# Performance work log

Hardware: AMD Instinct MI355X
Metric: run time of the kernel (lower is better)

Reference implementation:

```python
import jax, jax.numpy as jnp
import numpy as np

EPS = 1e-5  # torch LayerNorm default

def _ln(x, g, b):
    m = x.mean(-1, keepdims=True)
    v = x.var(-1, keepdims=True)  # biased var, matches torch LayerNorm
    return (x - m) * jax.lax.rsqrt(v + EPS) * g + b

def setup_inputs() -> dict:
    key = jax.random.key(0)
    ks = jax.random.split(key, 8)
    B, T, D, H, depth, C = 64, 512, 1024, 1024, 2, 1024
    return {
        'input': jax.random.normal(ks[0], (B, T, D), jnp.float32),
        'w_ih': jax.random.normal(ks[1], (depth, 4 * H, D), jnp.float32),
        'b_ih': jax.random.normal(ks[2], (depth, 4 * H), jnp.float32),
        'w_hh': jax.random.normal(ks[3], (depth, 4 * H, H), jnp.float32),
        'b_hh': jax.random.normal(ks[4], (depth, 4 * H), jnp.float32),
        'g_ih': jax.random.uniform(ks[5], (depth, 4 * H), jnp.float32),
        'be_ih': jnp.zeros((depth, 4 * H), jnp.float32),
        'g_hh': jax.random.uniform(ks[6], (depth, 4 * H), jnp.float32),
        'be_hh': jnp.zeros((depth, 4 * H), jnp.float32),
        'g_ho': jax.random.uniform(ks[7], (depth, H), jnp.float32),
        'be_ho': jnp.zeros((depth, H), jnp.float32),
        'fc_w': jax.random.normal(jax.random.fold_in(key, 9), (C, H), jnp.float32),
        'fc_b': jnp.zeros((C,), jnp.float32),
    }

def reference(input, w_ih, b_ih, w_hh, b_hh, g_ih, be_ih, g_hh, be_hh, g_ho, be_ho, fc_w, fc_b):
    B, T, D = input.shape
    depth, four_h, H = w_hh.shape
    H = four_h // 4
    h0 = jnp.zeros((depth, B, H), input.dtype)
    c0 = jnp.zeros((depth, B, H), input.dtype)
    xs = jnp.swapaxes(input, 0, 1)  # [T, B, D]

    def step(carry, x_t):
        h, c = carry
        x = x_t
        new_h, new_c = [], []
        for l in range(depth):  # small fixed layer loop
            gates = (_ln(x @ w_ih[l].T + b_ih[l], g_ih[l], be_ih[l])
                     + _ln(h[l] @ w_hh[l].T + b_hh[l], g_hh[l], be_hh[l]))  # [B, 4H]
            i, f, o = jnp.split(jax.nn.sigmoid(gates[:, :3 * H]), 3, axis=1)
            g = jnp.tanh(gates[:, 3 * H:])
            cy = f * c[l] + i * g
            hy = o * jnp.tanh(_ln(cy, g_ho[l], be_ho[l]))
            new_h.append(hy)
            new_c.append(cy)
            x = hy
        return (jnp.stack(new_h), jnp.stack(new_c)), x

    _, ys = jax.lax.scan(step, (h0, c0), xs)  # ys: [T, B, H] (top-layer h)
    out = jnp.swapaxes(ys, 0, 1).reshape(B * T, H) @ fc_w.T + fc_b
    return out.reshape(B, T, -1)
```

## Files before the change

### kernel.cpp

```cpp
#include <hip/hip_runtime.h>


typedef __attribute__((ext_vector_type(8))) short short8;
typedef __attribute__((ext_vector_type(8))) __bf16 bf16x8;
typedef __attribute__((ext_vector_type(4))) float f32x4;
typedef __attribute__((ext_vector_type(4))) unsigned short us4;

#define B_ 64
#define T_ 512
#define D_ 1024
#define H_ 1024
#define FH_ 4096
#define LAG_ 16
#define NS_ (T_ + LAG_)
#define RCH_ (B_ * 16)

typedef const __attribute__((address_space(1))) unsigned int* gas_ptr;
typedef __attribute__((address_space(3))) unsigned int* las_ptr;
#define GLOAD_LDS16(g, l) \
  __builtin_amdgcn_global_load_lds((gas_ptr)(g), (las_ptr)(l), 16, 0, 0)

static __device__ __forceinline__ unsigned short f2bf(float f) {
  unsigned int u = __builtin_bit_cast(unsigned int, f);
  u += 0x7FFFu + ((u >> 16) & 1u);
  return (unsigned short)(u >> 16);
}
static __device__ __forceinline__ float bf2f(unsigned short u) {
  unsigned int x = ((unsigned int)u) << 16;
  return __builtin_bit_cast(float, x);
}

__global__ void cast_split_k(const float4* __restrict__ in,
                             us4* __restrict__ hi, us4* __restrict__ lo, int n4) {
  int i = blockIdx.x * 256 + threadIdx.x;
  if (i < n4) {
    float4 v = in[i];
    us4 h, l;
    h[0] = f2bf(v.x); l[0] = f2bf(v.x - bf2f(h[0]));
    h[1] = f2bf(v.y); l[1] = f2bf(v.y - bf2f(h[1]));
    h[2] = f2bf(v.z); l[2] = f2bf(v.z - bf2f(h[2]));
    h[3] = f2bf(v.w); l[3] = f2bf(v.w - bf2f(h[3]));
    hi[i] = h; lo[i] = l;
  }
}

__global__ void transpose_split_k(const float4* __restrict__ x,
                                  us4* __restrict__ hi, us4* __restrict__ lo) {
  int i = blockIdx.x * 256 + threadIdx.x;
  int d4  = i & 255;
  int rem = i >> 8;
  int b = rem & 63;
  int t = rem >> 6;
  float4 v = x[((size_t)(b * T_ + t) << 8) + d4];
  us4 h, l;
  h[0] = f2bf(v.x); l[0] = f2bf(v.x - bf2f(h[0]));
  h[1] = f2bf(v.y); l[1] = f2bf(v.y - bf2f(h[1]));
  h[2] = f2bf(v.z); l[2] = f2bf(v.z - bf2f(h[2]));
  h[3] = f2bf(v.w); l[3] = f2bf(v.w - bf2f(h[3]));
  size_t o = ((size_t)(t * B_ + b) << 8) + d4;
  hi[o] = h; lo[o] = l;
}

__global__ void whh_frag_k(const float* __restrict__ w_hh,
                           unsigned short* __restrict__ frag) {
  int i = blockIdx.x * 256 + threadIdx.x;
  int sl   = i >> 12;
  int rem  = i & 4095;
  int sel  = rem >> 11;
  int kc   = (rem >> 6) & 31;
  int lane = rem & 63;
  int layer = sl >> 8, j = sl & 255;
  int col = j * 16 + (lane & 15);
  int kof = kc * 32 + (lane >> 4) * 8;
  const float* src = w_hh + ((size_t)layer * FH_ + col) * 1024 + kof;
  short8 o;
#pragma unroll
  for (int e = 0; e < 8; ++e) {
    float v = src[e];
    unsigned short h = f2bf(v);
    o[e] = sel ? (short)f2bf(v - bf2f(h)) : (short)h;
  }
  *(short8*)(frag + (size_t)i * 8) = o;
}

template <int FCMODE>
__global__ __launch_bounds__(256) void gemm3_k(
    const unsigned short* __restrict__ Ahi, const unsigned short* __restrict__ Alo,
    const unsigned short* __restrict__ Whi, const unsigned short* __restrict__ Wlo,
    const float* __restrict__ bias, float* __restrict__ out, int K, int N) {
  __shared__ unsigned short lAh[128 * 40];
  __shared__ unsigned short lAl[128 * 40];
  __shared__ unsigned short lWh[128 * 40];
  __shared__ unsigned short lWl[128 * 40];
  int tid = threadIdx.x;
  int l = tid & 63, w = tid >> 6;
  int r0 = blockIdx.y * 128, c0 = blockIdx.x * 128;
  int wr = (w >> 1) * 64, wc = (w & 1) * 64;
  int lr = l & 15, lk = (l >> 4) * 8;
  f32x4 acc[4][4] = {};
  int srow = tid >> 2;
  int scc  = (tid & 3) * 8;

  for (int kt = 0; kt < K; kt += 32) {
#pragma unroll
    for (int i = 0; i < 2; ++i) {
      int row = srow + i * 64;
      size_t aoff = (size_t)(r0 + row) * K + kt + scc;
      size_t woff = (size_t)(c0 + row) * K + kt + scc;
      *(short8*)&lAh[row * 40 + scc] = *(const short8*)(Ahi + aoff);
      *(short8*)&lAl[row * 40 + scc] = *(const short8*)(Alo + aoff);
      *(short8*)&lWh[row * 40 + scc] = *(const short8*)(Whi + woff);
      *(short8*)&lWl[row * 40 + scc] = *(const short8*)(Wlo + woff);
    }
    __syncthreads();
    bf16x8 ah[4], al[4], bh[4], bl[4];
#pragma unroll
    for (int mi = 0; mi < 4; ++mi) {
      ah[mi] = *(bf16x8*)&lAh[(wr + mi * 16 + lr) * 40 + lk];
      al[mi] = *(bf16x8*)&lAl[(wr + mi * 16 + lr) * 40 + lk];
    }
#pragma unroll
    for (int ni = 0; ni < 4; ++ni) {
      bh[ni] = *(bf16x8*)&lWh[(wc + ni * 16 + lr) * 40 + lk];
      bl[ni] = *(bf16x8*)&lWl[(wc + ni * 16 + lr) * 40 + lk];
    }
#pragma unroll
    for (int mi = 0; mi < 4; ++mi)
#pragma unroll
      for (int ni = 0; ni < 4; ++ni) {
        acc[mi][ni] = __builtin_amdgcn_mfma_f32_16x16x32_bf16(ah[mi], bh[ni], acc[mi][ni], 0, 0, 0);
        acc[mi][ni] = __builtin_amdgcn_mfma_f32_16x16x32_bf16(ah[mi], bl[ni], acc[mi][ni], 0, 0, 0);
        acc[mi][ni] = __builtin_amdgcn_mfma_f32_16x16x32_bf16(al[mi], bh[ni], acc[mi][ni], 0, 0, 0);
      }
    __syncthreads();
  }

#pragma unroll
  for (int mi = 0; mi < 4; ++mi)
#pragma unroll
    for (int ni = 0; ni < 4; ++ni)
#pragma unroll
      for (int reg = 0; reg < 4; ++reg) {
        int r = r0 + wr + mi * 16 + (l >> 4) * 4 + reg;
        int c = c0 + wc + ni * 16 + lr;
        float v = acc[mi][ni][reg] + bias[c];
        if (FCMODE) {
          int b = r & 63, t = r >> 6;
          out[((size_t)b * T_ + t) * (size_t)N + c] = v;
        } else {
          out[(size_t)r * N + c] = v;
        }
      }
}

__global__ __launch_bounds__(256) void hh_lds_k(
    const unsigned short* __restrict__ hH, const unsigned short* __restrict__ hL,
    const unsigned short* __restrict__ whhFrag,
    float* __restrict__ G, int s) {
  int layer = blockIdx.x >> 8;
  int t = layer ? (s - LAG_) : s;
  if (t < 0 || t >= T_) return;
  int j = blockIdx.x & 255;
  extern __shared__ char smem[];
  unsigned short* wl = (unsigned short*)smem;
  int tid = threadIdx.x;
  int l = tid & 63, w = tid >> 6;
  int lr = l & 15, lk = (l >> 4) * 8, lq = l >> 4;

  const unsigned short* gsrc = whhFrag + (((size_t)(layer * 256 + j)) << 15);
#pragma unroll
  for (int r = 0; r < 16; ++r) {
    int c = r * 256 + tid;
    GLOAD_LDS16(gsrc + (size_t)c * 8, wl + (size_t)(r * 256 + w * 64) * 8);
  }

  const unsigned short* hHb = hH + layer * 65536;
  const unsigned short* hLb = hL + layer * 65536;
  int m0 = w * 16;

  __syncthreads();

  f32x4 acc = {};
#pragma unroll 8
  for (int kc = 0; kc < 32; ++kc) {
    int k = kc * 32 + lk;
    bf16x8 ah = __builtin_bit_cast(bf16x8, *(const short8*)(hHb + (m0 + lr) * 1024 + k));
    bf16x8 al = __builtin_bit_cast(bf16x8, *(const short8*)(hLb + (m0 + lr) * 1024 + k));
    bf16x8 bh = __builtin_bit_cast(bf16x8, *(const short8*)&wl[(size_t)(kc * 64 + l) * 8]);
    bf16x8 bl = __builtin_bit_cast(bf16x8, *(const short8*)&wl[(size_t)(2048 + kc * 64 + l) * 8]);
    acc = __builtin_amdgcn_mfma_f32_16x16x32_bf16(ah, bh, acc, 0, 0, 0);
    acc = __builtin_amdgcn_mfma_f32_16x16x32_bf16(ah, bl, acc, 0, 0, 0);
    acc = __builtin_amdgcn_mfma_f32_16x16x32_bf16(al, bh, acc, 0, 0, 0);
  }
  float* Gb = G + layer * (64 * FH_);
  int n0 = j * 16;
#pragma unroll
  for (int reg = 0; reg < 4; ++reg) {
    int row = m0 + lq * 4 + reg;
    Gb[(size_t)row * FH_ + n0 + lr] = acc[reg];
  }
}

__device__ __forceinline__ void wave_red(float& v) {
#pragma unroll
  for (int o = 32; o; o >>= 1) v += __shfl_down(v, o);
}

__global__ __launch_bounds__(256) void pointwise_k(
    const float* __restrict__ P0, const float* __restrict__ P1,
    const float* __restrict__ G,
    const float* __restrict__ b_hh, const float* __restrict__ g_ih,
    const float* __restrict__ be_ih, const float* __restrict__ g_hh,
    const float* __restrict__ be_hh, const float* __restrict__ g_ho,
    const float* __restrict__ be_ho,
    float* __restrict__ cst,
    unsigned short* __restrict__ hH, unsigned short* __restrict__ hL,
    unsigned short* __restrict__ XYhi, unsigned short* __restrict__ XYlo,
    int s) {
  int layer = blockIdx.x >> 6;
  int t = layer ? (s - LAG_) : s;
  if (t < 0 || t >= T_) return;
  __shared__ float red[16];
  int r = blockIdx.x & 63, j = threadIdx.x;
  int wv = j >> 6, ln = j & 63;
  int slot = s & 15;
  const float* Pr = (layer ? P1 : P0) + ((size_t)slot * B_ + r) * FH_;
  const float* Gr = G + layer * (64 * FH_) + (size_t)r * FH_;
  const float* bhh = b_hh + layer * FH_;
  const float* gih = g_ih + layer * FH_;
  const float* beih= be_ih + layer * FH_;
  const float* ghh = g_hh + layer * FH_;
  const float* behh= be_hh + layer * FH_;
  const float* gho = g_ho + layer * H_;
  const float* beho= be_ho + layer * H_;
  float* crow = cst + layer * 65536 + (size_t)r * H_;

  float ihp[16], hhp[16];
  float s1 = 0, q1 = 0, s2 = 0, q2 = 0;
#pragma unroll
  for (int st = 0; st < 16; ++st) {
    int n = j + 256 * st;
    float a = Pr[n];
    float b = Gr[n] + bhh[n];
    ihp[st] = a; hhp[st] = b;
    s1 += a; q1 += a * a; s2 += b; q2 += b * b;
  }
  wave_red(s1); wave_red(q1); wave_red(s2); wave_red(q2);
  if (ln == 0) { red[wv * 4] = s1; red[wv * 4 + 1] = q1; red[wv * 4 + 2] = s2; red[wv * 4 + 3] = q2; }
  __syncthreads();
  s1 = red[0] + red[4] + red[8] + red[12];
  q1 = red[1] + red[5] + red[9] + red[13];
  s2 = red[2] + red[6] + red[10] + red[14];
  q2 = red[3] + red[7] + red[11] + red[15];
  __syncthreads();

  const float inv4h = 1.0f / 4096.0f;
  float m1 = s1 * inv4h, m2 = s2 * inv4h;
  float i1 = rsqrtf(q1 * inv4h - m1 * m1 + 1e-5f);
  float i2 = rsqrtf(q2 * inv4h - m2 * m2 + 1e-5f);

  float pre[16];
#pragma unroll
  for (int st = 0; st < 16; ++st) {
    int n = j + 256 * st;
    pre[st] = gih[n] * (ihp[st] - m1) * i1 + beih[n] + ghh[n] * (hhp[st] - m2) * i2 + behh[n];
  }

  float cn[4], og[4];
  float s3 = 0, q3 = 0;
#pragma unroll
  for (int u = 0; u < 4; ++u) {
    int hidx = j + 256 * u;
    float iG = 1.0f / (1.0f + __expf(-pre[u]));
    float fG = 1.0f / (1.0f + __expf(-pre[u + 4]));
    float oG = 1.0f / (1.0f + __expf(-pre[u + 8]));
    float gG = tanhf(pre[u + 12]);
    float c = fG * crow[hidx] + iG * gG;
    crow[hidx] = c;
    cn[u] = c; og[u] = oG;
    s3 += c; q3 += c * c;
  }
  wave_red(s3); wave_red(q3);
  if (ln == 0) { red[wv * 4] = s3; red[wv * 4 + 1] = q3; }
  __syncthreads();
  s3 = red[0] + red[4] + red[8] + red[12];
  q3 = red[1] + red[5] + red[9] + red[13];

  const float invh = 1.0f / 1024.0f;
  float m3 = s3 * invh;
  float i3 = rsqrtf(q3 * invh - m3 * m3 + 1e-5f);
  unsigned short* hHb = hH + layer * 65536 + (size_t)r * H_;
  unsigned short* hLb = hL + layer * 65536 + (size_t)r * H_;
  unsigned short* YH = XYhi + ((size_t)t * B_ + r) * H_;
  unsigned short* YL = XYlo + ((size_t)t * B_ + r) * H_;
#pragma unroll
  for (int u = 0; u < 4; ++u) {
    int hidx = j + 256 * u;
    float hy = og[u] * tanhf((cn[u] - m3) * i3 * gho[hidx] + beho[hidx]);
    unsigned short hv = f2bf(hy);
    unsigned short lv = f2bf(hy - bf2f(hv));
    hHb[hidx] = hv; hLb[hidx] = lv;
    YH[hidx] = hv;  YL[hidx] = lv;
  }
}

extern "C" void kernel_launch(void* const* d_in, const int* in_sizes, int n_in,
                              void* d_out, int out_size, void* d_ws, size_t ws_size,
                              hipStream_t stream) {
  const float* x    = (const float*)d_in[0];
  const float* w_ih = (const float*)d_in[1];
  const float* b_ih = (const float*)d_in[2];
  const float* w_hh = (const float*)d_in[3];
  const float* b_hh = (const float*)d_in[4];
  const float* g_ih = (const float*)d_in[5];
  const float* be_ih= (const float*)d_in[6];
  const float* g_hh = (const float*)d_in[7];
  const float* be_hh= (const float*)d_in[8];
  const float* g_ho = (const float*)d_in[9];
  const float* be_ho= (const float*)d_in[10];
  const float* fc_w = (const float*)d_in[11];
  const float* fc_b = (const float*)d_in[12];
  float* out = (float*)d_out;
  (void)ws_size; (void)in_sizes; (void)n_in; (void)out_size;

  char* wsb = (char*)d_ws;
  size_t off = 0;
  unsigned short* wihHi  = (unsigned short*)(wsb + off); off += 16777216;
  unsigned short* wihLo  = (unsigned short*)(wsb + off); off += 16777216;
  unsigned short* whhFrag= (unsigned short*)(wsb + off); off += 33554432;
  unsigned short* fcHi   = (unsigned short*)(wsb + off); off += 2097152;
  unsigned short* fcLo   = (unsigned short*)(wsb + off); off += 2097152;
  unsigned short* XYhi   = (unsigned short*)(wsb + off); off += 67108864;
  unsigned short* XYlo   = (unsigned short*)(wsb + off); off += 67108864;
  float* P0              = (float*)(wsb + off); off += (size_t)16 * B_ * FH_ * 4;
  float* P1              = (float*)(wsb + off); off += (size_t)16 * B_ * FH_ * 4;
  float* G               = (float*)(wsb + off); off += (size_t)2 * B_ * FH_ * 4;
  unsigned short* hH     = (unsigned short*)(wsb + off); off += 262144;
  unsigned short* hL     = (unsigned short*)(wsb + off); off += 262144;
  float* cst             = (float*)(wsb + off); off += 524288;

  {
    int n4 = 2 * FH_ * D_ / 4;
    cast_split_k<<<(n4 + 255) / 256, 256, 0, stream>>>((const float4*)w_ih, (us4*)wihHi, (us4*)wihLo, n4);
    int nf = H_ * H_ / 4;
    cast_split_k<<<(nf + 255) / 256, 256, 0, stream>>>((const float4*)fc_w, (us4*)fcHi, (us4*)fcLo, nf);
    int nx = T_ * B_ * D_ / 4;
    transpose_split_k<<<nx / 256, 256, 0, stream>>>((const float4*)x, (us4*)XYhi, (us4*)XYlo);
    whh_frag_k<<<8192, 256, 0, stream>>>(w_hh, whhFrag);
  }

  hipMemsetAsync(hH, 0, 262144, stream);
  hipMemsetAsync(hL, 0, 262144, stream);
  hipMemsetAsync(cst, 0, 524288, stream);

  hipFuncSetAttribute(reinterpret_cast<const void*>(hh_lds_k),
                      hipFuncAttributeMaxDynamicSharedMemorySize, 65536);

  for (int s = 0; s < NS_; ++s) {
    if ((s & 15) == 0) {
      if (s < T_) {
        gemm3_k<0><<<dim3(FH_ / 128, RCH_ / 128), 256, 0, stream>>>(
            XYhi + (size_t)s * B_ * D_, XYlo + (size_t)s * B_ * D_,
            wihHi, wihLo, b_ih, P0, D_, FH_);
      }
      if (s >= LAG_) {
        gemm3_k<0><<<dim3(FH_ / 128, RCH_ / 128), 256, 0, stream>>>(
            XYhi + (size_t)(s - LAG_) * B_ * D_, XYlo + (size_t)(s - LAG_) * B_ * D_,
            wihHi + (1 << 22), wihLo + (1 << 22), b_ih + FH_, P1, D_, FH_);
      }
    }
    hh_lds_k<<<512, 256, 65536, stream>>>(hH, hL, whhFrag, G, s);
    pointwise_k<<<128, 256, 0, stream>>>(P0, P1, G, b_hh, g_ih, be_ih, g_hh, be_hh,
                                         g_ho, be_ho, cst, hH, hL, XYhi, XYlo, s);
  }

  gemm3_k<1><<<dim3(H_ / 128, (T_ * B_) / 128), 256, 0, stream>>>(
      XYhi, XYlo, fcHi, fcLo, fc_b, out, H_, H_);
}
```

Measured before the change: 17.99 ms.

## Fuse recurrent matmul and pointwise LSTM step into one cooperative kernel

Replaces the per-step hh GEMM kernel and the pointwise LayerNorm/gate kernel with a single cooperative kernel of 256 blocks. Each block owns 8 hidden columns across all four gates, so the gate preactivations stay in LDS and the G buffer round trip disappears. Row LayerNorm statistics are combined across blocks with global atomics, separated by two software grid barriers. The intent is to remove one launch per step and the global traffic for G, at the cost of barrier spin latency, atomic contention, and a larger LDS footprint per block.

```diff
diff --git a/kernel.cpp b/kernel.cpp
--- a/kernel.cpp
+++ b/kernel.cpp
@@ -14,6 +14,9 @@
 #define LAG_ 16
 #define NS_ (T_ + LAG_)
 #define RCH_ (B_ * 16)
+
+#define SMEM_WHH 131072
+#define SMEM_TOTAL (SMEM_WHH + 64 * 33 * 4)
 
 typedef const __attribute__((address_space(1))) unsigned int* gas_ptr;
 typedef __attribute__((address_space(3))) unsigned int* las_ptr;
@@ -61,18 +64,19 @@
   hi[o] = h; lo[o] = l;
 }
 
-__global__ void whh_frag_k(const float* __restrict__ w_hh,
-                           unsigned short* __restrict__ frag) {
+__global__ void whh_frag3_k(const float* __restrict__ w_hh,
+                            unsigned short* __restrict__ frag) {
   int i = blockIdx.x * 256 + threadIdx.x;
-  int sl   = i >> 12;
-  int rem  = i & 4095;
-  int sel  = rem >> 11;
-  int kc   = (rem >> 6) & 31;
-  int lane = rem & 63;
-  int layer = sl >> 8, j = sl & 255;
-  int col = j * 16 + (lane & 15);
-  int kof = kc * 32 + (lane >> 4) * 8;
-  const float* src = w_hh + ((size_t)layer * FH_ + col) * 1024 + kof;
+  int lane = i & 63;
+  int kc   = (i >> 6) & 31;
+  int g    = (i >> 11) & 1;
+  int sel  = (i >> 12) & 1;
+  int j    = (i >> 13) & 127;
+  int layer= (i >> 20) & 1;
+  int fc = lane & 15;
+  int gc = (g * 2 + (fc >> 3)) * 1024 + j * 8 + (fc & 7);
+  int k0 = kc * 32 + (lane >> 4) * 8;
+  const float* src = w_hh + ((size_t)layer * FH_ + gc) * 1024 + k0;
   short8 o;
 #pragma unroll
   for (int e = 0; e < 8; ++e) {
@@ -153,154 +157,171 @@
       }
 }
 
-__global__ __launch_bounds__(256) void hh_lds_k(
-    const unsigned short* __restrict__ hH, const unsigned short* __restrict__ hL,
-    const unsigned short* __restrict__ whhFrag,
-    float* __restrict__ G, int s) {
-  int layer = blockIdx.x >> 8;
-  int t = layer ? (s - LAG_) : s;
-  if (t < 0 || t >= T_) return;
-  int j = blockIdx.x & 255;
+struct SP {
+  const unsigned short* whhF;
+  const float *P0, *P1;
+  unsigned short *hH, *hL, *XYhi, *XYlo;
+  float* cst;
+  const float *bhh, *gih, *beih, *ghh, *behh, *gho, *beho;
+  float *st1, *st2;
+  unsigned* cnt;
+  int s; unsigned tgt;
+};
+
+static __device__ __forceinline__ void gbar(unsigned* cnt, unsigned tgt, int tid) {
+  __syncthreads();
+  if (tid == 0) {
+    __threadfence();
+    atomicAdd(cnt, 1u);
+    while (__hip_atomic_load(cnt, __ATOMIC_RELAXED, __HIP_MEMORY_SCOPE_AGENT) < tgt)
+      __builtin_amdgcn_s_sleep(2);
+  }
+  __syncthreads();
+}
+
+__global__ __launch_bounds__(512) void fused_step_k(SP p) {
   extern __shared__ char smem[];
   unsigned short* wl = (unsigned short*)smem;
-  int tid = threadIdx.x;
-  int l = tid & 63, w = tid >> 6;
-  int lr = l & 15, lk = (l >> 4) * 8, lq = l >> 4;
-
-  const unsigned short* gsrc = whhFrag + (((size_t)(layer * 256 + j)) << 15);
-#pragma unroll
-  for (int r = 0; r < 16; ++r) {
-    int c = r * 256 + tid;
-    GLOAD_LDS16(gsrc + (size_t)c * 8, wl + (size_t)(r * 256 + w * 64) * 8);
-  }
-
-  const unsigned short* hHb = hH + layer * 65536;
-  const unsigned short* hLb = hL + layer * 65536;
-  int m0 = w * 16;
-
+  float* ldshh = (float*)(smem + SMEM_WHH);
+
+  const int tid = threadIdx.x;
+  const int blk = blockIdx.x;
+  const int layer = blk >> 7;
+  const int j = blk & 127;
+  const int t0 = layer ? (p.s - LAG_) : p.s;
+  const bool active = (t0 >= 0) && (t0 < T_);
+  const int l = tid & 63, w = tid >> 6;
+  const int lr = l & 15, lq = l >> 4;
+
+  if (active) {
+    const unsigned short* gsrc = p.whhF + (((size_t)(layer * 128 + j)) << 16);
+#pragma unroll
+    for (int r = 0; r < 16; ++r) {
+      int c = r * 512 + tid;
+      GLOAD_LDS16(gsrc + (size_t)c * 8, wl + (size_t)c * 8);
+    }
+  }
   __syncthreads();
 
-  f32x4 acc = {};
+  if (active) {
+    const int rf = w >> 1, g = w & 1;
+    const int rowbase = rf * 16;
+    const int fc = lr;
+    const int q = g * 2 + (fc >> 3);
+    const int gc = q * 1024 + j * 8 + (fc & 7);
+    const unsigned short* hHb = p.hH + layer * 65536;
+    const unsigned short* hLb = p.hL + layer * 65536;
+    f32x4 acc = {};
 #pragma unroll 8
-  for (int kc = 0; kc < 32; ++kc) {
-    int k = kc * 32 + lk;
-    bf16x8 ah = __builtin_bit_cast(bf16x8, *(const short8*)(hHb + (m0 + lr) * 1024 + k));
-    bf16x8 al = __builtin_bit_cast(bf16x8, *(const short8*)(hLb + (m0 + lr) * 1024 + k));
-    bf16x8 bh = __builtin_bit_cast(bf16x8, *(const short8*)&wl[(size_t)(kc * 64 + l) * 8]);
-    bf16x8 bl = __builtin_bit_cast(bf16x8, *(const short8*)&wl[(size_t)(2048 + kc * 64 + l) * 8]);
-    acc = __builtin_amdgcn_mfma_f32_16x16x32_bf16(ah, bh, acc, 0, 0, 0);
-    acc = __builtin_amdgcn_mfma_f32_16x16x32_bf16(ah, bl, acc, 0, 0, 0);
-    acc = __builtin_amdgcn_mfma_f32_16x16x32_bf16(al, bh, acc, 0, 0, 0);
-  }
-  float* Gb = G + layer * (64 * FH_);
-  int n0 = j * 16;
-#pragma unroll
-  for (int reg = 0; reg < 4; ++reg) {
-    int row = m0 + lq * 4 + reg;
-    Gb[(size_t)row * FH_ + n0 + lr] = acc[reg];
-  }
-}
-
-__device__ __forceinline__ void wave_red(float& v) {
-#pragma unroll
-  for (int o = 32; o; o >>= 1) v += __shfl_down(v, o);
-}
-
-__global__ __launch_bounds__(256) void pointwise_k(
-    const float* __restrict__ P0, const float* __restrict__ P1,
-    const float* __restrict__ G,
-    const float* __restrict__ b_hh, const float* __restrict__ g_ih,
-    const float* __restrict__ be_ih, const float* __restrict__ g_hh,
-    const float* __restrict__ be_hh, const float* __restrict__ g_ho,
-    const float* __restrict__ be_ho,
-    float* __restrict__ cst,
-    unsigned short* __restrict__ hH, unsigned short* __restrict__ hL,
-    unsigned short* __restrict__ XYhi, unsigned short* __restrict__ XYlo,
-    int s) {
-  int layer = blockIdx.x >> 6;
-  int t = layer ? (s - LAG_) : s;
-  if (t < 0 || t >= T_) return;
-  __shared__ float red[16];
-  int r = blockIdx.x & 63, j = threadIdx.x;
-  int wv = j >> 6, ln = j & 63;
-  int slot = s & 15;
-  const float* Pr = (layer ? P1 : P0) + ((size_t)slot * B_ + r) * FH_;
-  const float* Gr = G + layer * (64 * FH_) + (size_t)r * FH_;
-  const float* bhh = b_hh + layer * FH_;
-  const float* gih = g_ih + layer * FH_;
-  const float* beih= be_ih + layer * FH_;
-  const float* ghh = g_hh + layer * FH_;
-  const float* behh= be_hh + layer * FH_;
-  const float* gho = g_ho + layer * H_;
-  const float* beho= be_ho + layer * H_;
-  float* crow = cst + layer * 65536 + (size_t)r * H_;
-
-  float ihp[16], hhp[16];
-  float s1 = 0, q1 = 0, s2 = 0, q2 = 0;
-#pragma unroll
-  for (int st = 0; st < 16; ++st) {
-    int n = j + 256 * st;
-    float a = Pr[n];
-    float b = Gr[n] + bhh[n];
-    ihp[st] = a; hhp[st] = b;
-    s1 += a; q1 += a * a; s2 += b; q2 += b * b;
-  }
-  wave_red(s1); wave_red(q1); wave_red(s2); wave_red(q2);
-  if (ln == 0) { red[wv * 4] = s1; red[wv * 4 + 1] = q1; red[wv * 4 + 2] = s2; red[wv * 4 + 3] = q2; }
+    for (int kc = 0; kc < 32; ++kc) {
+      int k = kc * 32 + lq * 8;
+      bf16x8 ah = __builtin_bit_cast(bf16x8, *(const short8*)(hHb + (rowbase + lr) * 1024 + k));
+      bf16x8 al = __builtin_bit_cast(bf16x8, *(const short8*)(hLb + (rowbase + lr) * 1024 + k));
+      bf16x8 bh = __builtin_bit_cast(bf16x8, *(const short8*)&wl[(size_t)(g * 2048 + kc * 64 + l) * 8]);
+      bf16x8 bl = __builtin_bit_cast(bf16x8, *(const short8*)&wl[(size_t)(4096 + g * 2048 + kc * 64 + l) * 8]);
+      acc = __builtin_amdgcn_mfma_f32_16x16x32_bf16(ah, bh, acc, 0, 0, 0);
+      acc = __builtin_amdgcn_mfma_f32_16x16x32_bf16(al, bh, acc, 0, 0, 0);
+      acc = __builtin_amdgcn_mfma_f32_16x16x32_bf16(ah, bl, acc, 0, 0, 0);
+    }
+    float bhhv = p.bhh[layer * FH_ + gc];
+    int bc = q * 8 + (fc & 7);
+#pragma unroll
+    for (int reg = 0; reg < 4; ++reg)
+      ldshh[(rowbase + lq * 4 + reg) * 33 + bc] = acc[reg] + bhhv;
+  }
   __syncthreads();
-  s1 = red[0] + red[4] + red[8] + red[12];
-  q1 = red[1] + red[5] + red[9] + red[13];
-  s2 = red[2] + red[6] + red[10] + red[14];
-  q2 = red[3] + red[7] + red[11] + red[15];
-  __syncthreads();
-
-  const float inv4h = 1.0f / 4096.0f;
-  float m1 = s1 * inv4h, m2 = s2 * inv4h;
-  float i1 = rsqrtf(q1 * inv4h - m1 * m1 + 1e-5f);
-  float i2 = rsqrtf(q2 * inv4h - m2 * m2 + 1e-5f);
-
-  float pre[16];
-#pragma unroll
-  for (int st = 0; st < 16; ++st) {
-    int n = j + 256 * st;
-    pre[st] = gih[n] * (ihp[st] - m1) * i1 + beih[n] + ghh[n] * (hhp[st] - m2) * i2 + behh[n];
-  }
-
-  float cn[4], og[4];
-  float s3 = 0, q3 = 0;
-#pragma unroll
-  for (int u = 0; u < 4; ++u) {
-    int hidx = j + 256 * u;
-    float iG = 1.0f / (1.0f + __expf(-pre[u]));
-    float fG = 1.0f / (1.0f + __expf(-pre[u + 4]));
-    float oG = 1.0f / (1.0f + __expf(-pre[u + 8]));
-    float gG = tanhf(pre[u + 12]);
-    float c = fG * crow[hidx] + iG * gG;
-    crow[hidx] = c;
-    cn[u] = c; og[u] = oG;
-    s3 += c; q3 += c * c;
-  }
-  wave_red(s3); wave_red(q3);
-  if (ln == 0) { red[wv * 4] = s3; red[wv * 4 + 1] = q3; }
-  __syncthreads();
-  s3 = red[0] + red[4] + red[8] + red[12];
-  q3 = red[1] + red[5] + red[9] + red[13];
-
-  const float invh = 1.0f / 1024.0f;
-  float m3 = s3 * invh;
-  float i3 = rsqrtf(q3 * invh - m3 * m3 + 1e-5f);
-  unsigned short* hHb = hH + layer * 65536 + (size_t)r * H_;
-  unsigned short* hLb = hL + layer * 65536 + (size_t)r * H_;
-  unsigned short* YH = XYhi + ((size_t)t * B_ + r) * H_;
-  unsigned short* YL = XYlo + ((size_t)t * B_ + r) * H_;
-#pragma unroll
-  for (int u = 0; u < 4; ++u) {
-    int hidx = j + 256 * u;
-    float hy = og[u] * tanhf((cn[u] - m3) * i3 * gho[hidx] + beho[hidx]);
+
+  const int row = tid >> 3, c8 = tid & 7;
+  const int hcol = j * 8 + c8;
+  const int par = p.s & 1;
+  float* st1 = p.st1 + ((size_t)par * 2 + layer) * 256;
+  float* st2 = p.st2 + ((size_t)par * 2 + layer) * 128;
+  float ih[4], hh[4];
+  if (active) {
+    const float* Pb = layer ? p.P1 : p.P0;
+    int slot = p.s & 15;
+    float s1 = 0, q1 = 0, s2 = 0, q2 = 0;
+#pragma unroll
+    for (int q = 0; q < 4; ++q) {
+      float a = Pb[((size_t)(slot * B_ + row)) * FH_ + q * 1024 + hcol];
+      float b = ldshh[row * 33 + q * 8 + c8];
+      ih[q] = a; hh[q] = b;
+      s1 += a; q1 += a * a; s2 += b; q2 += b * b;
+    }
+#pragma unroll
+    for (int off = 1; off < 8; off <<= 1) {
+      s1 += __shfl_xor(s1, off); q1 += __shfl_xor(q1, off);
+      s2 += __shfl_xor(s2, off); q2 += __shfl_xor(q2, off);
+    }
+    if (c8 == 0) {
+      atomicAdd(&st1[row * 4 + 0], s1);
+      atomicAdd(&st1[row * 4 + 1], q1);
+      atomicAdd(&st1[row * 4 + 2], s2);
+      atomicAdd(&st1[row * 4 + 3], q2);
+    }
+  }
+  gbar(p.cnt, p.tgt, tid);
+
+  float cv = 0.0f, ogate = 0.0f;
+  if (active) {
+    float S1 = __hip_atomic_load(&st1[row * 4 + 0], __ATOMIC_RELAXED, __HIP_MEMORY_SCOPE_AGENT);
+    float Q1 = __hip_atomic_load(&st1[row * 4 + 1], __ATOMIC_RELAXED, __HIP_MEMORY_SCOPE_AGENT);
+    float S2 = __hip_atomic_load(&st1[row * 4 + 2], __ATOMIC_RELAXED, __HIP_MEMORY_SCOPE_AGENT);
+    float Q2 = __hip_atomic_load(&st1[row * 4 + 3], __ATOMIC_RELAXED, __HIP_MEMORY_SCOPE_AGENT);
+    const float inv4h = 1.0f / 4096.0f;
+    float m1 = S1 * inv4h, m2 = S2 * inv4h;
+    float i1 = rsqrtf(Q1 * inv4h - m1 * m1 + 1e-5f);
+    float i2 = rsqrtf(Q2 * inv4h - m2 * m2 + 1e-5f);
+    float pre[4];
+#pragma unroll
+    for (int q = 0; q < 4; ++q) {
+      int gc = layer * FH_ + q * 1024 + hcol;
+      pre[q] = p.gih[gc] * (ih[q] - m1) * i1 + p.beih[gc]
+             + p.ghh[gc] * (hh[q] - m2) * i2 + p.behh[gc];
+    }
+    float iG = 1.0f / (1.0f + __expf(-pre[0]));
+    float fG = 1.0f / (1.0f + __expf(-pre[1]));
+    float oG = 1.0f / (1.0f + __expf(-pre[2]));
+    float gG = tanhf(pre[3]);
+    size_t cidx = ((size_t)(layer * B_ + row)) * H_ + hcol;
+    cv = fG * p.cst[cidx] + iG * gG;
+    p.cst[cidx] = cv;
+    ogate = oG;
+    float sc = cv, sq = cv * cv;
+#pragma unroll
+    for (int off = 1; off < 8; off <<= 1) {
+      sc += __shfl_xor(sc, off); sq += __shfl_xor(sq, off);
+    }
+    if (c8 == 0) {
+      atomicAdd(&st2[row * 2 + 0], sc);
+      atomicAdd(&st2[row * 2 + 1], sq);
+    }
+  }
+  gbar(p.cnt + 1, p.tgt, tid);
+
+  if (active) {
+    float S3 = __hip_atomic_load(&st2[row * 2 + 0], __ATOMIC_RELAXED, __HIP_MEMORY_SCOPE_AGENT);
+    float Q3 = __hip_atomic_load(&st2[row * 2 + 1], __ATOMIC_RELAXED, __HIP_MEMORY_SCOPE_AGENT);
+    const float invh = 1.0f / 1024.0f;
+    float m3 = S3 * invh;
+    float i3 = rsqrtf(Q3 * invh - m3 * m3 + 1e-5f);
+    int hidx = layer * H_ + hcol;
+    float hy = ogate * tanhf((cv - m3) * i3 * p.gho[hidx] + p.beho[hidx]);
     unsigned short hv = f2bf(hy);
     unsigned short lv = f2bf(hy - bf2f(hv));
-    hHb[hidx] = hv; hLb[hidx] = lv;
-    YH[hidx] = hv;  YL[hidx] = lv;
+    size_t ho = ((size_t)(layer * B_ + row)) * H_ + hcol;
+    p.hH[ho] = hv; p.hL[ho] = lv;
+    size_t yo = ((size_t)t0 * B_ + row) * H_ + hcol;
+    p.XYhi[yo] = hv; p.XYlo[yo] = lv;
+  }
+
+  if (blk == 0) {
+    int op = (p.s + 1) & 1;
+    float* z1 = p.st1 + (size_t)op * 512;
+    float* z2 = p.st2 + (size_t)op * 256;
+    __hip_atomic_store(&z1[tid], 0.0f, __ATOMIC_RELAXED, __HIP_MEMORY_SCOPE_AGENT);
+    if (tid < 256)
+      __hip_atomic_store(&z2[tid], 0.0f, __ATOMIC_RELAXED, __HIP_MEMORY_SCOPE_AGENT);
   }
 }
 
@@ -327,17 +348,19 @@
   size_t off = 0;
   unsigned short* wihHi  = (unsigned short*)(wsb + off); off += 16777216;
   unsigned short* wihLo  = (unsigned short*)(wsb + off); off += 16777216;
-  unsigned short* whhFrag= (unsigned short*)(wsb + off); off += 33554432;
+  unsigned short* whhF   = (unsigned short*)(wsb + off); off += 33554432;
   unsigned short* fcHi   = (unsigned short*)(wsb + off); off += 2097152;
   unsigned short* fcLo   = (unsigned short*)(wsb + off); off += 2097152;
   unsigned short* XYhi   = (unsigned short*)(wsb + off); off += 67108864;
   unsigned short* XYlo   = (unsigned short*)(wsb + off); off += 67108864;
   float* P0              = (float*)(wsb + off); off += (size_t)16 * B_ * FH_ * 4;
   float* P1              = (float*)(wsb + off); off += (size_t)16 * B_ * FH_ * 4;
-  float* G               = (float*)(wsb + off); off += (size_t)2 * B_ * FH_ * 4;
   unsigned short* hH     = (unsigned short*)(wsb + off); off += 262144;
   unsigned short* hL     = (unsigned short*)(wsb + off); off += 262144;
   float* cst             = (float*)(wsb + off); off += 524288;
+  float* st1             = (float*)(wsb + off); off += 4096;
+  float* st2             = (float*)(wsb + off); off += 2048;
+  unsigned* cnt          = (unsigned*)(wsb + off); off += 256;
 
   {
     int n4 = 2 * FH_ * D_ / 4;
@@ -346,15 +369,24 @@
     cast_split_k<<<(nf + 255) / 256, 256, 0, stream>>>((const float4*)fc_w, (us4*)fcHi, (us4*)fcLo, nf);
     int nx = T_ * B_ * D_ / 4;
     transpose_split_k<<<nx / 256, 256, 0, stream>>>((const float4*)x, (us4*)XYhi, (us4*)XYlo);
-    whh_frag_k<<<8192, 256, 0, stream>>>(w_hh, whhFrag);
+    whh_frag3_k<<<8192, 256, 0, stream>>>(w_hh, whhF);
   }
 
   hipMemsetAsync(hH, 0, 262144, stream);
   hipMemsetAsync(hL, 0, 262144, stream);
   hipMemsetAsync(cst, 0, 524288, stream);
-
-  hipFuncSetAttribute(reinterpret_cast<const void*>(hh_lds_k),
-                      hipFuncAttributeMaxDynamicSharedMemorySize, 65536);
+  hipMemsetAsync(st1, 0, 4096 + 2048 + 256, stream);
+
+  hipFuncSetAttribute(reinterpret_cast<const void*>(fused_step_k),
+                      hipFuncAttributeMaxDynamicSharedMemorySize, SMEM_TOTAL);
+
+  SP prm;
+  prm.whhF = whhF; prm.P0 = P0; prm.P1 = P1;
+  prm.hH = hH; prm.hL = hL; prm.XYhi = XYhi; prm.XYlo = XYlo;
+  prm.cst = cst;
+  prm.bhh = b_hh; prm.gih = g_ih; prm.beih = be_ih;
+  prm.ghh = g_hh; prm.behh = be_hh; prm.gho = g_ho; prm.beho = be_ho;
+  prm.st1 = st1; prm.st2 = st2; prm.cnt = cnt;
 
   for (int s = 0; s < NS_; ++s) {
     if ((s & 15) == 0) {
@@ -369,9 +401,11 @@
             wihHi + (1 << 22), wihLo + (1 << 22), b_ih + FH_, P1, D_, FH_);
       }
     }
-    hh_lds_k<<<512, 256, 65536, stream>>>(hH, hL, whhFrag, G, s);
-    pointwise_k<<<128, 256, 0, stream>>>(P0, P1, G, b_hh, g_ih, be_ih, g_hh, be_hh,
-                                         g_ho, be_ho, cst, hH, hL, XYhi, XYlo, s);
+    prm.s = s;
+    prm.tgt = 256u * (unsigned)(s + 1);
+    void* args[] = { &prm };
+    hipLaunchCooperativeKernel(reinterpret_cast<void*>(fused_step_k),
+                               dim3(256), dim3(512), args, SMEM_TOTAL, stream);
   }
 
   gemm3_k<1><<<dim3(H_ / 128, (T_ * B_) / 128), 256, 0, stream>>>(
```

New measurement: 45.69 ms. +154.0%, slower.

## Fuse recurrent GEMM and pointwise into persistent span kernel with flag barriers

Applied to the files above, without the earlier changes.

Replaces the per-timestep pair of launches (hh GEMM plus pointwise) with one persistent kernel per 16-step span. Each of 256 blocks keeps its slice of W_hh resident in 128KB of LDS and synchronises through a software grid barrier built on global flags. The cell state stays in registers across the span. This removes about a thousand kernel launches and the repeated W_hh reloads into LDS. The cost is a busy-wait barrier twice per step, and it relies on all 256 blocks being co-resident, which risks deadlock if they are not.

```diff
diff --git a/kernel.cpp b/kernel.cpp
--- a/kernel.cpp
+++ b/kernel.cpp
@@ -12,8 +12,11 @@
 #define H_ 1024
 #define FH_ 4096
 #define LAG_ 16
-#define NS_ (T_ + LAG_)
+#define NSPAN 16
+#define SPANS 33
 #define RCH_ (B_ * 16)
+
+#define SMEM_WHH 131072
 
 typedef const __attribute__((address_space(1))) unsigned int* gas_ptr;
 typedef __attribute__((address_space(3))) unsigned int* las_ptr;
@@ -64,13 +67,16 @@
 __global__ void whh_frag_k(const float* __restrict__ w_hh,
                            unsigned short* __restrict__ frag) {
   int i = blockIdx.x * 256 + threadIdx.x;
-  int sl   = i >> 12;
-  int rem  = i & 4095;
-  int sel  = rem >> 11;
-  int kc   = (rem >> 6) & 31;
-  int lane = rem & 63;
-  int layer = sl >> 8, j = sl & 255;
-  int col = j * 16 + (lane & 15);
+  int b    = i >> 13;
+  int rem  = i & 8191;
+  int sel  = rem >> 12;
+  int rem2 = rem & 4095;
+  int g    = rem2 >> 11;
+  int rem3 = rem2 & 2047;
+  int kc   = rem3 >> 6;
+  int lane = rem3 & 63;
+  int layer = b >> 7;
+  int col = (b & 127) * 32 + g * 16 + (lane & 15);
   int kof = kc * 32 + (lane >> 4) * 8;
   const float* src = w_hh + ((size_t)layer * FH_ + col) * 1024 + kof;
   short8 o;
@@ -153,154 +159,212 @@
       }
 }
 
-__global__ __launch_bounds__(256) void hh_lds_k(
-    const unsigned short* __restrict__ hH, const unsigned short* __restrict__ hL,
-    const unsigned short* __restrict__ whhFrag,
-    float* __restrict__ G, int s) {
-  int layer = blockIdx.x >> 8;
-  int t = layer ? (s - LAG_) : s;
-  if (t < 0 || t >= T_) return;
-  int j = blockIdx.x & 255;
+struct SpanP {
+  const unsigned short* whhF;
+  const float *P0, *P1;
+  unsigned short *hH, *hL, *XYhi, *XYlo;
+  float *cst, *G;
+  const float *bhh, *gih, *beih, *ghh, *behh, *gho, *beho;
+  unsigned* flags;
+  int s0; unsigned ep0;
+};
+
+static __device__ __forceinline__ void flagbar(unsigned* flags, unsigned ep,
+                                               int tid, unsigned* bmin) {
+  __syncthreads();
+  if (tid == 0) {
+    __threadfence();
+    __hip_atomic_store(&flags[blockIdx.x], ep, __ATOMIC_RELAXED,
+                       __HIP_MEMORY_SCOPE_AGENT);
+  }
+  const int w = tid >> 6, l = tid & 63;
+  for (;;) {
+    unsigned v = __hip_atomic_load(&flags[((w & 3) << 6) | l], __ATOMIC_RELAXED,
+                                   __HIP_MEMORY_SCOPE_AGENT);
+#pragma unroll
+    for (int o = 32; o; o >>= 1) {
+      unsigned u = (unsigned)__shfl_xor((int)v, o);
+      v = v < u ? v : u;
+    }
+    if (l == 0) bmin[w] = v;
+    __syncthreads();
+    unsigned m = bmin[0];
+#pragma unroll
+    for (int k = 1; k < 8; ++k) { unsigned u = bmin[k]; m = m < u ? m : u; }
+    if (m >= ep) break;
+    __syncthreads();
+    __builtin_amdgcn_s_sleep(4);
+  }
+  if (tid == 0) __threadfence();
+  __syncthreads();
+}
+
+__global__ __launch_bounds__(512) void span_k(SpanP p) {
   extern __shared__ char smem[];
   unsigned short* wl = (unsigned short*)smem;
-  int tid = threadIdx.x;
-  int l = tid & 63, w = tid >> 6;
-  int lr = l & 15, lk = (l >> 4) * 8, lq = l >> 4;
-
-  const unsigned short* gsrc = whhFrag + (((size_t)(layer * 256 + j)) << 15);
-#pragma unroll
-  for (int r = 0; r < 16; ++r) {
-    int c = r * 256 + tid;
-    GLOAD_LDS16(gsrc + (size_t)c * 8, wl + (size_t)(r * 256 + w * 64) * 8);
-  }
-
-  const unsigned short* hHb = hH + layer * 65536;
-  const unsigned short* hLb = hL + layer * 65536;
-  int m0 = w * 16;
-
-  __syncthreads();
-
-  f32x4 acc = {};
+  __shared__ float red[32];
+  __shared__ unsigned bmin[8];
+
+  const int tid = threadIdx.x;
+  const int blk = blockIdx.x;
+  const int w = tid >> 6, l = tid & 63;
+  const int lr = l & 15, lq = l >> 4;
+
+  {
+    const unsigned short* gsrc = p.whhF + ((size_t)blk << 16);
+#pragma unroll
+    for (int r = 0; r < 16; ++r) {
+      int c = r * 512 + tid;
+      GLOAD_LDS16(gsrc + (size_t)c * 8, wl + (size_t)c * 8);
+    }
+    __syncthreads();
+  }
+
+  const int pw_layer = blk >> 6;
+  const int pw_r = blk & 63;
+  float creg[2] = {0.0f, 0.0f};
+  if (blk < 128) {
+#pragma unroll
+    for (int u = 0; u < 2; ++u)
+      creg[u] = p.cst[((size_t)(pw_layer * B_ + pw_r)) * H_ + tid + 512 * u];
+  }
+
+  unsigned ep = p.ep0;
+  for (int sl = 0; sl < NSPAN; ++sl) {
+    int s = p.s0 + sl;
+
+    {
+      int layer = blk >> 7;
+      int t0 = layer ? (s - LAG_) : s;
+      if (t0 >= 0 && t0 < T_) {
+        int jb = blk & 127;
+        int cf = w >> 2;
+        int m0 = (w & 3) * 16;
+        const unsigned short* hHb = p.hH + layer * 65536;
+        const unsigned short* hLb = p.hL + layer * 65536;
+        const short8* wfrag = (const short8*)wl;
+        f32x4 acc = {};
 #pragma unroll 8
-  for (int kc = 0; kc < 32; ++kc) {
-    int k = kc * 32 + lk;
-    bf16x8 ah = __builtin_bit_cast(bf16x8, *(const short8*)(hHb + (m0 + lr) * 1024 + k));
-    bf16x8 al = __builtin_bit_cast(bf16x8, *(const short8*)(hLb + (m0 + lr) * 1024 + k));
-    bf16x8 bh = __builtin_bit_cast(bf16x8, *(const short8*)&wl[(size_t)(kc * 64 + l) * 8]);
-    bf16x8 bl = __builtin_bit_cast(bf16x8, *(const short8*)&wl[(size_t)(2048 + kc * 64 + l) * 8]);
-    acc = __builtin_amdgcn_mfma_f32_16x16x32_bf16(ah, bh, acc, 0, 0, 0);
-    acc = __builtin_amdgcn_mfma_f32_16x16x32_bf16(ah, bl, acc, 0, 0, 0);
-    acc = __builtin_amdgcn_mfma_f32_16x16x32_bf16(al, bh, acc, 0, 0, 0);
-  }
-  float* Gb = G + layer * (64 * FH_);
-  int n0 = j * 16;
-#pragma unroll
-  for (int reg = 0; reg < 4; ++reg) {
-    int row = m0 + lq * 4 + reg;
-    Gb[(size_t)row * FH_ + n0 + lr] = acc[reg];
-  }
-}
-
-__device__ __forceinline__ void wave_red(float& v) {
-#pragma unroll
-  for (int o = 32; o; o >>= 1) v += __shfl_down(v, o);
-}
-
-__global__ __launch_bounds__(256) void pointwise_k(
-    const float* __restrict__ P0, const float* __restrict__ P1,
-    const float* __restrict__ G,
-    const float* __restrict__ b_hh, const float* __restrict__ g_ih,
-    const float* __restrict__ be_ih, const float* __restrict__ g_hh,
-    const float* __restrict__ be_hh, const float* __restrict__ g_ho,
-    const float* __restrict__ be_ho,
-    float* __restrict__ cst,
-    unsigned short* __restrict__ hH, unsigned short* __restrict__ hL,
-    unsigned short* __restrict__ XYhi, unsigned short* __restrict__ XYlo,
-    int s) {
-  int layer = blockIdx.x >> 6;
-  int t = layer ? (s - LAG_) : s;
-  if (t < 0 || t >= T_) return;
-  __shared__ float red[16];
-  int r = blockIdx.x & 63, j = threadIdx.x;
-  int wv = j >> 6, ln = j & 63;
-  int slot = s & 15;
-  const float* Pr = (layer ? P1 : P0) + ((size_t)slot * B_ + r) * FH_;
-  const float* Gr = G + layer * (64 * FH_) + (size_t)r * FH_;
-  const float* bhh = b_hh + layer * FH_;
-  const float* gih = g_ih + layer * FH_;
-  const float* beih= be_ih + layer * FH_;
-  const float* ghh = g_hh + layer * FH_;
-  const float* behh= be_hh + layer * FH_;
-  const float* gho = g_ho + layer * H_;
-  const float* beho= be_ho + layer * H_;
-  float* crow = cst + layer * 65536 + (size_t)r * H_;
-
-  float ihp[16], hhp[16];
-  float s1 = 0, q1 = 0, s2 = 0, q2 = 0;
-#pragma unroll
-  for (int st = 0; st < 16; ++st) {
-    int n = j + 256 * st;
-    float a = Pr[n];
-    float b = Gr[n] + bhh[n];
-    ihp[st] = a; hhp[st] = b;
-    s1 += a; q1 += a * a; s2 += b; q2 += b * b;
-  }
-  wave_red(s1); wave_red(q1); wave_red(s2); wave_red(q2);
-  if (ln == 0) { red[wv * 4] = s1; red[wv * 4 + 1] = q1; red[wv * 4 + 2] = s2; red[wv * 4 + 3] = q2; }
-  __syncthreads();
-  s1 = red[0] + red[4] + red[8] + red[12];
-  q1 = red[1] + red[5] + red[9] + red[13];
-  s2 = red[2] + red[6] + red[10] + red[14];
-  q2 = red[3] + red[7] + red[11] + red[15];
-  __syncthreads();
-
-  const float inv4h = 1.0f / 4096.0f;
-  float m1 = s1 * inv4h, m2 = s2 * inv4h;
-  float i1 = rsqrtf(q1 * inv4h - m1 * m1 + 1e-5f);
-  float i2 = rsqrtf(q2 * inv4h - m2 * m2 + 1e-5f);
-
-  float pre[16];
-#pragma unroll
-  for (int st = 0; st < 16; ++st) {
-    int n = j + 256 * st;
-    pre[st] = gih[n] * (ihp[st] - m1) * i1 + beih[n] + ghh[n] * (hhp[st] - m2) * i2 + behh[n];
-  }
-
-  float cn[4], og[4];
-  float s3 = 0, q3 = 0;
-#pragma unroll
-  for (int u = 0; u < 4; ++u) {
-    int hidx = j + 256 * u;
-    float iG = 1.0f / (1.0f + __expf(-pre[u]));
-    float fG = 1.0f / (1.0f + __expf(-pre[u + 4]));
-    float oG = 1.0f / (1.0f + __expf(-pre[u + 8]));
-    float gG = tanhf(pre[u + 12]);
-    float c = fG * crow[hidx] + iG * gG;
-    crow[hidx] = c;
-    cn[u] = c; og[u] = oG;
-    s3 += c; q3 += c * c;
-  }
-  wave_red(s3); wave_red(q3);
-  if (ln == 0) { red[wv * 4] = s3; red[wv * 4 + 1] = q3; }
-  __syncthreads();
-  s3 = red[0] + red[4] + red[8] + red[12];
-  q3 = red[1] + red[5] + red[9] + red[13];
-
-  const float invh = 1.0f / 1024.0f;
-  float m3 = s3 * invh;
-  float i3 = rsqrtf(q3 * invh - m3 * m3 + 1e-5f);
-  unsigned short* hHb = hH + layer * 65536 + (size_t)r * H_;
-  unsigned short* hLb = hL + layer * 65536 + (size_t)r * H_;
-  unsigned short* YH = XYhi + ((size_t)t * B_ + r) * H_;
-  unsigned short* YL = XYlo + ((size_t)t * B_ + r) * H_;
-#pragma unroll
-  for (int u = 0; u < 4; ++u) {
-    int hidx = j + 256 * u;
-    float hy = og[u] * tanhf((cn[u] - m3) * i3 * gho[hidx] + beho[hidx]);
-    unsigned short hv = f2bf(hy);
-    unsigned short lv = f2bf(hy - bf2f(hv));
-    hHb[hidx] = hv; hLb[hidx] = lv;
-    YH[hidx] = hv;  YL[hidx] = lv;
+        for (int kc = 0; kc < 32; ++kc) {
+          int k = kc * 32 + lq * 8;
+          bf16x8 ah = __builtin_bit_cast(bf16x8, *(const short8*)(hHb + (m0 + lr) * 1024 + k));
+          bf16x8 al = __builtin_bit_cast(bf16x8, *(const short8*)(hLb + (m0 + lr) * 1024 + k));
+          bf16x8 bh = __builtin_bit_cast(bf16x8, wfrag[(cf * 32 + kc) * 64 + l]);
+          bf16x8 bl = __builtin_bit_cast(bf16x8, wfrag[4096 + (cf * 32 + kc) * 64 + l]);
+          acc = __builtin_amdgcn_mfma_f32_16x16x32_bf16(ah, bh, acc, 0, 0, 0);
+          acc = __builtin_amdgcn_mfma_f32_16x16x32_bf16(al, bh, acc, 0, 0, 0);
+          acc = __builtin_amdgcn_mfma_f32_16x16x32_bf16(ah, bl, acc, 0, 0, 0);
+        }
+        float* Gb = p.G + layer * (64 * FH_);
+        int n0 = jb * 32 + cf * 16;
+#pragma unroll
+        for (int reg = 0; reg < 4; ++reg) {
+          int row = m0 + lq * 4 + reg;
+          Gb[(size_t)row * FH_ + n0 + lr] = acc[reg];
+        }
+      }
+    }
+    ++ep; flagbar(p.flags, ep, tid, bmin);
+
+    if (blk < 128) {
+      int layer = pw_layer;
+      int t0 = layer ? (s - LAG_) : s;
+      if (t0 >= 0 && t0 < T_) {
+        int r = pw_r;
+        int slot = s & 15;
+        const float* Pr = (layer ? p.P1 : p.P0) + ((size_t)slot * B_ + r) * FH_;
+        const float* Gr = p.G + layer * (64 * FH_) + (size_t)r * FH_;
+        const float* bhh = p.bhh + layer * FH_;
+        const float* gih = p.gih + layer * FH_;
+        const float* beih= p.beih + layer * FH_;
+        const float* ghh = p.ghh + layer * FH_;
+        const float* behh= p.behh + layer * FH_;
+        const float* gho = p.gho + layer * H_;
+        const float* beho= p.beho + layer * H_;
+        int wv = tid >> 6, ln = tid & 63;
+
+        float ihp[8], hhp[8];
+        float s1 = 0, q1 = 0, s2 = 0, q2 = 0;
+#pragma unroll
+        for (int st = 0; st < 8; ++st) {
+          int n = tid + 512 * st;
+          float a = Pr[n];
+          float b = Gr[n] + bhh[n];
+          ihp[st] = a; hhp[st] = b;
+          s1 += a; q1 += a * a; s2 += b; q2 += b * b;
+        }
+#pragma unroll
+        for (int o = 32; o; o >>= 1) {
+          s1 += __shfl_down(s1, o); q1 += __shfl_down(q1, o);
+          s2 += __shfl_down(s2, o); q2 += __shfl_down(q2, o);
+        }
+        if (ln == 0) { red[wv*4] = s1; red[wv*4+1] = q1; red[wv*4+2] = s2; red[wv*4+3] = q2; }
+        __syncthreads();
+        s1 = 0; q1 = 0; s2 = 0; q2 = 0;
+#pragma unroll
+        for (int k = 0; k < 8; ++k) {
+          s1 += red[k*4]; q1 += red[k*4+1]; s2 += red[k*4+2]; q2 += red[k*4+3];
+        }
+        __syncthreads();
+
+        const float inv4h = 1.0f / 4096.0f;
+        float m1 = s1 * inv4h, m2 = s2 * inv4h;
+        float i1 = rsqrtf(q1 * inv4h - m1 * m1 + 1e-5f);
+        float i2 = rsqrtf(q2 * inv4h - m2 * m2 + 1e-5f);
+
+        float pre[8];
+#pragma unroll
+        for (int st = 0; st < 8; ++st) {
+          int n = tid + 512 * st;
+          pre[st] = gih[n] * (ihp[st] - m1) * i1 + beih[n] + ghh[n] * (hhp[st] - m2) * i2 + behh[n];
+        }
+
+        float cn[2], og[2];
+        float s3 = 0, q3 = 0;
+#pragma unroll
+        for (int u = 0; u < 2; ++u) {
+          float iG = 1.0f / (1.0f + __expf(-pre[u]));
+          float fG = 1.0f / (1.0f + __expf(-pre[2 + u]));
+          float oG = 1.0f / (1.0f + __expf(-pre[4 + u]));
+          float gG = tanhf(pre[6 + u]);
+          float c = fG * creg[u] + iG * gG;
+          creg[u] = c;
+          cn[u] = c; og[u] = oG;
+          s3 += c; q3 += c * c;
+        }
+#pragma unroll
+        for (int o = 32; o; o >>= 1) { s3 += __shfl_down(s3, o); q3 += __shfl_down(q3, o); }
+        if (ln == 0) { red[wv*4] = s3; red[wv*4+1] = q3; }
+        __syncthreads();
+        s3 = 0; q3 = 0;
+#pragma unroll
+        for (int k = 0; k < 8; ++k) { s3 += red[k*4]; q3 += red[k*4+1]; }
+
+        const float invh = 1.0f / 1024.0f;
+        float m3 = s3 * invh;
+        float i3 = rsqrtf(q3 * invh - m3 * m3 + 1e-5f);
+        unsigned short* hHb = p.hH + layer * 65536 + (size_t)r * H_;
+        unsigned short* hLb = p.hL + layer * 65536 + (size_t)r * H_;
+        unsigned short* YH = p.XYhi + ((size_t)t0 * B_ + r) * H_;
+        unsigned short* YL = p.XYlo + ((size_t)t0 * B_ + r) * H_;
+#pragma unroll
+        for (int u = 0; u < 2; ++u) {
+          int hidx = tid + 512 * u;
+          float hy = og[u] * tanhf((cn[u] - m3) * i3 * gho[hidx] + beho[hidx]);
+          unsigned short hv = f2bf(hy);
+          unsigned short lv = f2bf(hy - bf2f(hv));
+          hHb[hidx] = hv; hLb[hidx] = lv;
+          YH[hidx] = hv;  YL[hidx] = lv;
+        }
+      }
+    }
+    if (sl < NSPAN - 1) { ++ep; flagbar(p.flags, ep, tid, bmin); }
+  }
+
+  if (blk < 128) {
+#pragma unroll
+    for (int u = 0; u < 2; ++u)
+      p.cst[((size_t)(pw_layer * B_ + pw_r)) * H_ + tid + 512 * u] = creg[u];
   }
 }
 
@@ -327,7 +391,7 @@
   size_t off = 0;
   unsigned short* wihHi  = (unsigned short*)(wsb + off); off += 16777216;
   unsigned short* wihLo  = (unsigned short*)(wsb + off); off += 16777216;
-  unsigned short* whhFrag= (unsigned short*)(wsb + off); off += 33554432;
+  unsigned short* whhF   = (unsigned short*)(wsb + off); off += 33554432;
   unsigned short* fcHi   = (unsigned short*)(wsb + off); off += 2097152;
   unsigned short* fcLo   = (unsigned short*)(wsb + off); off += 2097152;
   unsigned short* XYhi   = (unsigned short*)(wsb + off); off += 67108864;
@@ -338,6 +402,7 @@
   unsigned short* hH     = (unsigned short*)(wsb + off); off += 262144;
   unsigned short* hL     = (unsigned short*)(wsb + off); off += 262144;
   float* cst             = (float*)(wsb + off); off += 524288;
+  unsigned* flags        = (unsigned*)(wsb + off); off += 1024;
 
   {
     int n4 = 2 * FH_ * D_ / 4;
@@ -346,32 +411,40 @@
     cast_split_k<<<(nf + 255) / 256, 256, 0, stream>>>((const float4*)fc_w, (us4*)fcHi, (us4*)fcLo, nf);
     int nx = T_ * B_ * D_ / 4;
     transpose_split_k<<<nx / 256, 256, 0, stream>>>((const float4*)x, (us4*)XYhi, (us4*)XYlo);
-    whh_frag_k<<<8192, 256, 0, stream>>>(w_hh, whhFrag);
+    whh_frag_k<<<8192, 256, 0, stream>>>(w_hh, whhF);
   }
 
   hipMemsetAsync(hH, 0, 262144, stream);
   hipMemsetAsync(hL, 0, 262144, stream);
   hipMemsetAsync(cst, 0, 524288, stream);
-
-  hipFuncSetAttribute(reinterpret_cast<const void*>(hh_lds_k),
-                      hipFuncAttributeMaxDynamicSharedMemorySize, 65536);
-
-  for (int s = 0; s < NS_; ++s) {
-    if ((s & 15) == 0) {
-      if (s < T_) {
-        gemm3_k<0><<<dim3(FH_ / 128, RCH_ / 128), 256, 0, stream>>>(
-            XYhi + (size_t)s * B_ * D_, XYlo + (size_t)s * B_ * D_,
-            wihHi, wihLo, b_ih, P0, D_, FH_);
-      }
-      if (s >= LAG_) {
-        gemm3_k<0><<<dim3(FH_ / 128, RCH_ / 128), 256, 0, stream>>>(
-            XYhi + (size_t)(s - LAG_) * B_ * D_, XYlo + (size_t)(s - LAG_) * B_ * D_,
-            wihHi + (1 << 22), wihLo + (1 << 22), b_ih + FH_, P1, D_, FH_);
-      }
-    }
-    hh_lds_k<<<512, 256, 65536, stream>>>(hH, hL, whhFrag, G, s);
-    pointwise_k<<<128, 256, 0, stream>>>(P0, P1, G, b_hh, g_ih, be_ih, g_hh, be_hh,
-                                         g_ho, be_ho, cst, hH, hL, XYhi, XYlo, s);
+  hipMemsetAsync(flags, 0, 1024, stream);
+
+  hipFuncSetAttribute(reinterpret_cast<const void*>(span_k),
+                      hipFuncAttributeMaxDynamicSharedMemorySize, SMEM_WHH);
+
+  SpanP prm;
+  prm.whhF = whhF; prm.P0 = P0; prm.P1 = P1;
+  prm.hH = hH; prm.hL = hL; prm.XYhi = XYhi; prm.XYlo = XYlo;
+  prm.cst = cst; prm.G = G;
+  prm.bhh = b_hh; prm.gih = g_ih; prm.beih = be_ih;
+  prm.ghh = g_hh; prm.behh = be_hh; prm.gho = g_ho; prm.beho = be_ho;
+  prm.flags = flags;
+
+  for (int c = 0; c < SPANS; ++c) {
+    int s = c * NSPAN;
+    if (s < T_) {
+      gemm3_k<0><<<dim3(FH_ / 128, RCH_ / 128), 256, 0, stream>>>(
+          XYhi + (size_t)s * B_ * D_, XYlo + (size_t)s * B_ * D_,
+          wihHi, wihLo, b_ih, P0, D_, FH_);
+    }
+    if (s >= LAG_) {
+      gemm3_k<0><<<dim3(FH_ / 128, RCH_ / 128), 256, 0, stream>>>(
+          XYhi + (size_t)(s - LAG_) * B_ * D_, XYlo + (size_t)(s - LAG_) * B_ * D_,
+          wihHi + (1 << 22), wihLo + (1 << 22), b_ih + FH_, P1, D_, FH_);
+    }
+    prm.s0 = s;
+    prm.ep0 = (unsigned)c * 31u;
+    span_k<<<256, 512, SMEM_WHH, stream>>>(prm);
   }
 
   gemm3_k<1><<<dim3(H_ / 128, (T_ * B_) / 128), 256, 0, stream>>>(
```

Measured after the change: 33.97 ms. 88.8% more time.
